# Kernel tuning notes

Measured on AMD Instinct MI355X. Metric: run time of the kernel, lower is better.

## Reference

```python
import jax, jax.numpy as jnp
import numpy as np

TOP_K = 2
NUM_EXPERTS = 8


def setup_inputs() -> dict:
    key = jax.random.key(0)
    ks = jax.random.split(key, 5)
    N, D, H, E = 32768, 1024, 1024, NUM_EXPERTS
    s = 1.0 / np.sqrt(D)
    return {
        "x": jax.random.normal(ks[0], (N, D), dtype=jnp.float32),
        "router_w": jax.random.normal(ks[1], (E, D), dtype=jnp.float32) * s,
        "router_b": jax.random.normal(ks[2], (E,), dtype=jnp.float32) * s,
        "expert_w": jax.random.normal(ks[3], (E, D, H), dtype=jnp.float32) * s,
        "expert_b": jax.random.normal(ks[4], (E, H), dtype=jnp.float32) * s,
    }


def reference(x, router_w, router_b, expert_w, expert_b):
    # Router: torch Linear -> x @ W.T + b ; logits [N, E]
    logits = x @ router_w.T + router_b
    vals, idx = jax.lax.top_k(logits, TOP_K)          # [N, K]
    w = jax.nn.softmax(vals, axis=-1)                  # softmax over top-k values
    # combine[n, e] = sum of top-k weights routed to expert e (0 if not chosen)
    combine = jnp.sum(jax.nn.one_hot(idx, NUM_EXPERTS, dtype=x.dtype) * w[..., None], axis=1)  # [N, E]
    # Accumulate weighted expert outputs; unchosen tokens get combine==0,
    # which matches the torch masking (bias excluded for unchosen tokens).
    out = jnp.zeros((x.shape[0], expert_w.shape[2]), dtype=x.dtype)
    for e in range(NUM_EXPERTS):
        out = out + combine[:, e:e + 1] * (x @ expert_w[e] + expert_b[e])
    return out
```

## Files before the change

### kernel.cpp

```cpp
#include <hip/hip_runtime.h>
#include <hip/hip_bf16.h>
#include <math.h>

#define N_TOK 32768
#define DIM   1024
#define HID   1024
#define NE    8
#define GX    64

typedef __bf16 bf16_t;
typedef __bf16 bf16x8 __attribute__((ext_vector_type(8)));
typedef __bf16 bf16x4 __attribute__((ext_vector_type(4)));
typedef float  f32x4  __attribute__((ext_vector_type(4)));

#define GLOAD_LDS(g, s) __builtin_amdgcn_global_load_lds(                      \
    (const __attribute__((address_space(1))) void*)(g),                        \
    (__attribute__((address_space(3))) void*)(s), 16, 0, 0)

__global__ __launch_bounds__(256) void convert_w_kernel(const float* __restrict__ W,
                                                        bf16_t* __restrict__ Wt) {
  __shared__ float tile[64][65];
  const int e  = blockIdx.z;
  const int d0 = blockIdx.x * 64;
  const int h0 = blockIdx.y * 64;
  const int t  = threadIdx.x;
  const float* src = W + (size_t)e * DIM * HID;
#pragma unroll
  for (int p = 0; p < 4; ++p) {
    int r = p * 16 + (t >> 4);
    int c = (t & 15) * 4;
    f32x4 v = *(const f32x4*)&src[(size_t)(d0 + r) * HID + h0 + c];
    tile[r][c + 0] = v[0]; tile[r][c + 1] = v[1];
    tile[r][c + 2] = v[2]; tile[r][c + 3] = v[3];
  }
  __syncthreads();
  const int hr = t >> 2, dseg = t & 3;
  bf16_t tmp[16];
#pragma unroll
  for (int j = 0; j < 16; ++j) tmp[j] = (bf16_t)tile[dseg * 16 + j][hr];
  bf16_t* dst = Wt + (size_t)e * HID * DIM + (size_t)(h0 + hr) * DIM + d0 + dseg * 16;
  *(bf16x8*)dst       = *(const bf16x8*)tmp;
  *(bf16x8*)(dst + 8) = *(const bf16x8*)(tmp + 8);
}

__global__ __launch_bounds__(256) void router_kernel(
    const float* __restrict__ x, const float* __restrict__ rw,
    const float* __restrict__ rb, bf16_t* __restrict__ xb,
    int* __restrict__ tok_list, float* __restrict__ w_list,
    int* __restrict__ gcnt) {
  __shared__ float rws[NE * DIM];
  __shared__ int   ce0[64], ce1[64];
  __shared__ float cw0[64], cw1[64];
  __shared__ int   lp0[64], lp1[64];
  __shared__ int   lcnt[2 * NE], gbase[2 * NE];
  const int t = threadIdx.x;
#pragma unroll
  for (int p = 0; p < 8; ++p) {
    int i4 = p * 256 + t;
    *(f32x4*)&rws[i4 * 4] = *(const f32x4*)&rw[i4 * 4];
  }
  if (t < 2 * NE) lcnt[t] = 0;
  __syncthreads();

  const int w = t >> 6, l = t & 63, ts = l >> 4, sub = l & 15;
  const int base = blockIdx.x * 64;
  for (int it = 0; it < 4; ++it) {
    const int lt    = it * 16 + w * 4 + ts;
    const int token = base + lt;
    const float* xrow  = x  + (size_t)token * DIM;
    bf16_t*      xbrow = xb + (size_t)token * DIM;
    double acc[NE];
#pragma unroll
    for (int e = 0; e < NE; ++e) acc[e] = 0.0;
    for (int p = 0; p < 16; ++p) {
      const int d = p * 64 + sub * 4;
      f32x4 xv = *(const f32x4*)&xrow[d];
      bf16x4 bv;
#pragma unroll
      for (int j = 0; j < 4; ++j) bv[j] = (bf16_t)xv[j];
      *(bf16x4*)&xbrow[d] = bv;
#pragma unroll
      for (int e = 0; e < NE; ++e) {
        f32x4 rv = *(const f32x4*)&rws[e * DIM + d];
        acc[e] += (double)xv[0] * (double)rv[0] + (double)xv[1] * (double)rv[1]
                + (double)xv[2] * (double)rv[2] + (double)xv[3] * (double)rv[3];
      }
    }
#pragma unroll
    for (int e = 0; e < NE; ++e) {
      double v = acc[e];
      v += __shfl_xor(v, 1, 16);
      v += __shfl_xor(v, 2, 16);
      v += __shfl_xor(v, 4, 16);
      v += __shfl_xor(v, 8, 16);
      acc[e] = v;
    }
    if (sub == 0) {
      double lv[NE];
#pragma unroll
      for (int e = 0; e < NE; ++e) lv[e] = acc[e] + (double)rb[e];
      int e0 = 0; double v0 = lv[0];
#pragma unroll
      for (int e = 1; e < NE; ++e) if (lv[e] > v0) { v0 = lv[e]; e0 = e; }
      int e1 = -1; double v1 = -1.0e300;
#pragma unroll
      for (int e = 0; e < NE; ++e) if (e != e0 && lv[e] > v1) { v1 = lv[e]; e1 = e; }
      const float ef = expf((float)(v1 - v0));
      const float s  = 1.0f + ef;
      ce0[lt] = e0; ce1[lt] = e1;
      cw0[lt] = 1.0f / s; cw1[lt] = ef / s;
    }
  }
  __syncthreads();
  if (t < 64) {
    lp0[t] = atomicAdd(&lcnt[ce0[t] * 2 + 0], 1);
    lp1[t] = atomicAdd(&lcnt[ce1[t] * 2 + 1], 1);
  }
  __syncthreads();
  if (t < 2 * NE) gbase[t] = atomicAdd(&gcnt[t], lcnt[t]);
  __syncthreads();
  if (t < 64) {
    const int token = base + t;
    const int le0 = ce0[t] * 2 + 0, le1 = ce1[t] * 2 + 1;
    const int p0 = gbase[le0] + lp0[t];
    const int p1 = gbase[le1] + lp1[t];
    tok_list[le0 * N_TOK + p0] = token;  w_list[le0 * N_TOK + p0] = cw0[t];
    tok_list[le1 * N_TOK + p1] = token;  w_list[le1 * N_TOK + p1] = cw1[t];
  }
}

#define BM 128
#define BN 128
#define BK 32

__global__ __launch_bounds__(256) void moe_gemm_kernel(
    const bf16_t* __restrict__ xb, const bf16_t* __restrict__ wt,
    const float* __restrict__ eb, const int* __restrict__ tok_list,
    const float* __restrict__ w_list, const int* __restrict__ gcnt,
    float* __restrict__ out, int slot) {
  const int f  = blockIdx.x + GX * (blockIdx.y + (HID / BN) * blockIdx.z);
  const int wg = (f & 7) * (GX * (HID / BN) * NE / 8) + (f >> 3);
  const int bx = wg % GX;
  const int by = (wg / GX) % (HID / BN);
  const int e  = wg / (GX * (HID / BN));

  const int le = e * 2 + slot;
  const int c  = gcnt[le];
  const int m0 = bx * BM;
  if (m0 >= c) return;
  const int h0 = by * BN;

  __shared__ bf16_t As[BM * BK];
  __shared__ bf16_t Bs[BN * BK];
  __shared__ int    tok_s[BM];
  __shared__ float  w_s[BM];

  const int t = threadIdx.x;
  if (t < BM) {
    int r  = m0 + t;
    int rc = r < c ? r : c - 1;
    tok_s[t] = tok_list[le * N_TOK + rc];
    w_s[t]   = (r < c) ? w_list[le * N_TOK + r] : 0.0f;
  }
  __syncthreads();

  const int w  = t >> 6, l = t & 63;
  const int wr = w >> 1, wc = w & 1;
  const int srow = t >> 2, sslot = t & 3;
  const int sx = (sslot ^ (srow & 3)) * 8;

  const bf16_t* ag0 = xb + (size_t)tok_s[srow] * DIM + sx;
  const bf16_t* ag1 = xb + (size_t)tok_s[srow + 64] * DIM + sx;
  const bf16_t* wbase = wt + (size_t)e * HID * DIM;
  const bf16_t* bg0 = wbase + (size_t)(h0 + srow) * DIM + sx;
  const bf16_t* bg1 = wbase + (size_t)(h0 + srow + 64) * DIM + sx;

  f32x4 acc[4][4];
  const f32x4 fzero = {0.0f, 0.0f, 0.0f, 0.0f};
#pragma unroll
  for (int m = 0; m < 4; ++m)
#pragma unroll
    for (int n = 0; n < 4; ++n) acc[m][n] = fzero;

  const int fr = l & 15, fq = l >> 4;
  const int rdx = (fq ^ (fr & 3)) * 8;

  for (int k0 = 0; k0 < DIM; k0 += BK) {
    GLOAD_LDS(ag0 + k0, As + w * 512);
    GLOAD_LDS(ag1 + k0, As + 2048 + w * 512);
    GLOAD_LDS(bg0 + k0, Bs + w * 512);
    GLOAD_LDS(bg1 + k0, Bs + 2048 + w * 512);
    __syncthreads();

    bf16x8 af[4], bfg[4];
#pragma unroll
    for (int m = 0; m < 4; ++m)
      af[m] = *(const bf16x8*)&As[(wr * 64 + m * 16 + fr) * BK + rdx];
#pragma unroll
    for (int n = 0; n < 4; ++n)
      bfg[n] = *(const bf16x8*)&Bs[(wc * 64 + n * 16 + fr) * BK + rdx];
#pragma unroll
    for (int m = 0; m < 4; ++m)
#pragma unroll
      for (int n = 0; n < 4; ++n)
        acc[m][n] = __builtin_amdgcn_mfma_f32_16x16x32_bf16(af[m], bfg[n],
                                                            acc[m][n], 0, 0, 0);
    __syncthreads();
  }

#pragma unroll
  for (int n = 0; n < 4; ++n) {
    const int h    = h0 + wc * 64 + n * 16 + fr;
    const float bias = eb[e * HID + h];
#pragma unroll
    for (int m = 0; m < 4; ++m) {
#pragma unroll
      for (int q = 0; q < 4; ++q) {
        const int r  = wr * 64 + m * 16 + fq * 4 + q;
        const float wv = w_s[r];
        if (wv != 0.0f) {
          const size_t o = (size_t)tok_s[r] * HID + h;
          const float  v = wv * (acc[m][n][q] + bias);
          if (slot == 0) out[o] = v;
          else           out[o] = out[o] + v;
        }
      }
    }
  }
}

extern "C" void kernel_launch(void* const* d_in, const int* in_sizes, int n_in,
                              void* d_out, int out_size, void* d_ws, size_t ws_size,
                              hipStream_t stream) {
  const float* x  = (const float*)d_in[0];
  const float* rw = (const float*)d_in[1];
  const float* rb = (const float*)d_in[2];
  const float* ew = (const float*)d_in[3];
  const float* eb = (const float*)d_in[4];
  float* out = (float*)d_out;

  char* ws = (char*)d_ws;
  bf16_t* xb       = (bf16_t*)(ws);
  bf16_t* wt       = (bf16_t*)(ws + 67108864);
  int*    tok_list = (int*)   (ws + 83886080);
  float*  w_list   = (float*) (ws + 85983232);
  int*    gcnt     = (int*)   (ws + 88080384);

  hipMemsetAsync(gcnt, 0, 2 * NE * sizeof(int), stream);

  convert_w_kernel<<<dim3(DIM / 64, HID / 64, NE), 256, 0, stream>>>(ew, wt);
  router_kernel<<<dim3(N_TOK / 64), 256, 0, stream>>>(x, rw, rb, xb,
                                                      tok_list, w_list, gcnt);

  dim3 grid(GX, HID / BN, NE);
  moe_gemm_kernel<<<grid, 256, 0, stream>>>(xb, wt, eb, tok_list, w_list, gcnt,
                                            out, 0);
  moe_gemm_kernel<<<grid, 256, 0, stream>>>(xb, wt, eb, tok_list, w_list, gcnt,
                                            out, 1);
}
```

Baseline: 577.8 us.

## Enlarge MoE GEMM tiles to 256x256 with a double-buffered async LDS pipeline

Rewrites the grouped expert GEMM to use 256x256 output tiles with BK=64, 512 threads and a 128KB dynamic LDS double buffer. Async global-to-LDS loads are issued in quarter-tile steps ahead of the MFMA work and tracked with explicit vmcnt waits and raw barriers. s_setprio is raised around the MFMA bursts. The aim is more data reuse per tile and less load latency exposed between k-steps. The cost is higher register and LDS pressure, and only one workgroup may fit per CU.

```diff
diff --git a/kernel.cpp b/kernel.cpp
--- a/kernel.cpp
+++ b/kernel.cpp
@@ -6,7 +6,6 @@
 #define DIM   1024
 #define HID   1024
 #define NE    8
-#define GX    64
 
 typedef __bf16 bf16_t;
 typedef __bf16 bf16x8 __attribute__((ext_vector_type(8)));
@@ -16,6 +15,9 @@
 #define GLOAD_LDS(g, s) __builtin_amdgcn_global_load_lds(                      \
     (const __attribute__((address_space(1))) void*)(g),                        \
     (__attribute__((address_space(3))) void*)(s), 16, 0, 0)
+
+#define BARRIER() do { __builtin_amdgcn_s_barrier();                           \
+                       asm volatile("" ::: "memory"); } while (0)
 
 __global__ __launch_bounds__(256) void convert_w_kernel(const float* __restrict__ W,
                                                         bf16_t* __restrict__ Wt) {
@@ -129,20 +131,39 @@
   }
 }
 
-#define BM 128
-#define BN 128
-#define BK 32
-
-__global__ __launch_bounds__(256) void moe_gemm_kernel(
+#define BM 256
+#define BN 256
+#define BK 64
+#define NT (DIM / BK)
+#define GX 32
+
+#define MF(x, y, m, n) acc[m][n] = \
+    __builtin_amdgcn_mfma_f32_16x16x32_bf16((x), (y), acc[m][n], 0, 0, 0)
+
+#define MFMA16(MB) do {                                                        \
+    __builtin_amdgcn_s_setprio(1);                                             \
+    MF(a0, b0, (MB)+0, 0); MF(a0, b1, (MB)+0, 1);                              \
+    MF(a0, b2, (MB)+0, 2); MF(a0, b3, (MB)+0, 3);                              \
+    MF(a1, b0, (MB)+1, 0); MF(a1, b1, (MB)+1, 1);                              \
+    MF(a1, b2, (MB)+1, 2); MF(a1, b3, (MB)+1, 3);                              \
+    MF(a2, b0, (MB)+2, 0); MF(a2, b1, (MB)+2, 1);                              \
+    MF(a2, b2, (MB)+2, 2); MF(a2, b3, (MB)+2, 3);                              \
+    MF(a3, b0, (MB)+3, 0); MF(a3, b1, (MB)+3, 1);                              \
+    MF(a3, b2, (MB)+3, 2); MF(a3, b3, (MB)+3, 3);                              \
+    __builtin_amdgcn_s_setprio(0);                                             \
+  } while (0)
+
+__global__ __launch_bounds__(512, 2) void moe_gemm_kernel(
     const bf16_t* __restrict__ xb, const bf16_t* __restrict__ wt,
     const float* __restrict__ eb, const int* __restrict__ tok_list,
     const float* __restrict__ w_list, const int* __restrict__ gcnt,
     float* __restrict__ out, int slot) {
-  const int f  = blockIdx.x + GX * (blockIdx.y + (HID / BN) * blockIdx.z);
+  const int f  = blockIdx.x;
   const int wg = (f & 7) * (GX * (HID / BN) * NE / 8) + (f >> 3);
-  const int bx = wg % GX;
-  const int by = (wg / GX) % (HID / BN);
   const int e  = wg / (GX * (HID / BN));
+  const int rr = wg % (GX * (HID / BN));
+  const int bx = rr >> 2;
+  const int by = rr & 3;
 
   const int le = e * 2 + slot;
   const int c  = gcnt[le];
@@ -150,10 +171,9 @@
   if (m0 >= c) return;
   const int h0 = by * BN;
 
-  __shared__ bf16_t As[BM * BK];
-  __shared__ bf16_t Bs[BN * BK];
-  __shared__ int    tok_s[BM];
-  __shared__ float  w_s[BM];
+  extern __shared__ bf16_t lds[];
+  __shared__ int   tok_s[BM];
+  __shared__ float w_s[BM];
 
   const int t = threadIdx.x;
   if (t < BM) {
@@ -164,63 +184,118 @@
   }
   __syncthreads();
 
+  const int srow = t >> 2, sslot = t & 3;
+  const int sswz = (sslot ^ ((srow >> 1) & 3)) * 8;
+  const bf16_t* wbase = wt + (size_t)e * HID * DIM;
+  const bf16_t* aR0 = xb + (size_t)tok_s[srow] * DIM + sswz;
+  const bf16_t* aR1 = xb + (size_t)tok_s[srow + 128] * DIM + sswz;
+  const bf16_t* bR0 = wbase + (size_t)(h0 + srow) * DIM + sswz;
+  const bf16_t* bR1 = wbase + (size_t)(h0 + srow + 128) * DIM + sswz;
+
+  auto stage_half = [&](int s_) {
+    if (s_ < 4 * NT) {
+      const int tile_ = s_ >> 2;
+      const int typ_  = s_ & 3;
+      const int buf_  = tile_ & 1;
+      const int kk_   = typ_ >> 1;
+      const int koff_ = tile_ * BK + kk_ * 32;
+      bf16_t* db_ = lds + ((typ_ & 1) ? 32768 : 0) + buf_ * 16384 + kk_ * 8192
+                        + t * 8;
+      if (typ_ & 1) { GLOAD_LDS(bR0 + koff_, db_); GLOAD_LDS(bR1 + koff_, db_ + 4096); }
+      else          { GLOAD_LDS(aR0 + koff_, db_); GLOAD_LDS(aR1 + koff_, db_ + 4096); }
+    }
+  };
+
   const int w  = t >> 6, l = t & 63;
-  const int wr = w >> 1, wc = w & 1;
-  const int srow = t >> 2, sslot = t & 3;
-  const int sx = (sslot ^ (srow & 3)) * 8;
-
-  const bf16_t* ag0 = xb + (size_t)tok_s[srow] * DIM + sx;
-  const bf16_t* ag1 = xb + (size_t)tok_s[srow + 64] * DIM + sx;
-  const bf16_t* wbase = wt + (size_t)e * HID * DIM;
-  const bf16_t* bg0 = wbase + (size_t)(h0 + srow) * DIM + sx;
-  const bf16_t* bg1 = wbase + (size_t)(h0 + srow + 64) * DIM + sx;
-
-  f32x4 acc[4][4];
+  const int wr = w >> 2, wc = w & 3;
+  const int fr = l & 15, fq = l >> 4;
+  const int rswz = (fq ^ ((fr >> 1) & 3)) * 8;
+  const int aoff = (wr * 128 + fr) * 32 + rswz;
+  const int boff = (wc * 64 + fr) * 32 + rswz;
+
+  f32x4 acc[8][4];
   const f32x4 fzero = {0.0f, 0.0f, 0.0f, 0.0f};
 #pragma unroll
-  for (int m = 0; m < 4; ++m)
+  for (int m = 0; m < 8; ++m)
 #pragma unroll
     for (int n = 0; n < 4; ++n) acc[m][n] = fzero;
 
-  const int fr = l & 15, fq = l >> 4;
-  const int rdx = (fq ^ (fr & 3)) * 8;
-
-  for (int k0 = 0; k0 < DIM; k0 += BK) {
-    GLOAD_LDS(ag0 + k0, As + w * 512);
-    GLOAD_LDS(ag1 + k0, As + 2048 + w * 512);
-    GLOAD_LDS(bg0 + k0, Bs + w * 512);
-    GLOAD_LDS(bg1 + k0, Bs + 2048 + w * 512);
-    __syncthreads();
-
-    bf16x8 af[4], bfg[4];
-#pragma unroll
-    for (int m = 0; m < 4; ++m)
-      af[m] = *(const bf16x8*)&As[(wr * 64 + m * 16 + fr) * BK + rdx];
-#pragma unroll
-    for (int n = 0; n < 4; ++n)
-      bfg[n] = *(const bf16x8*)&Bs[(wc * 64 + n * 16 + fr) * BK + rdx];
-#pragma unroll
-    for (int m = 0; m < 4; ++m)
-#pragma unroll
-      for (int n = 0; n < 4; ++n)
-        acc[m][n] = __builtin_amdgcn_mfma_f32_16x16x32_bf16(af[m], bfg[n],
-                                                            acc[m][n], 0, 0, 0);
-    __syncthreads();
-  }
-
-#pragma unroll
-  for (int n = 0; n < 4; ++n) {
-    const int h    = h0 + wc * 64 + n * 16 + fr;
+  stage_half(0); stage_half(1); stage_half(2); stage_half(3);
+  stage_half(4); stage_half(5); stage_half(6);
+  asm volatile("s_waitcnt vmcnt(6)" ::: "memory");
+  BARRIER();
+  int s = 7;
+
+#pragma unroll 2
+  for (int kt = 0; kt < NT; ++kt) {
+    const int buf = kt & 1;
+    const bf16_t* Ab0 = lds + buf * 16384;
+    const bf16_t* Ab1 = Ab0 + 8192;
+    const bf16_t* Bb0 = lds + 32768 + buf * 16384;
+    const bf16_t* Bb1 = Bb0 + 8192;
+    bf16x8 a0, a1, a2, a3, b0, b1, b2, b3;
+
+    a0 = *(const bf16x8*)(Ab0 + aoff + 0 * 512);
+    a1 = *(const bf16x8*)(Ab0 + aoff + 1 * 512);
+    a2 = *(const bf16x8*)(Ab0 + aoff + 2 * 512);
+    a3 = *(const bf16x8*)(Ab0 + aoff + 3 * 512);
+    b0 = *(const bf16x8*)(Bb0 + boff + 0 * 512);
+    b1 = *(const bf16x8*)(Bb0 + boff + 1 * 512);
+    b2 = *(const bf16x8*)(Bb0 + boff + 2 * 512);
+    b3 = *(const bf16x8*)(Bb0 + boff + 3 * 512);
+    stage_half(s + 0);
+    BARRIER();
+    MFMA16(0);
+    BARRIER();
+
+    a0 = *(const bf16x8*)(Ab0 + aoff + 4 * 512);
+    a1 = *(const bf16x8*)(Ab0 + aoff + 5 * 512);
+    a2 = *(const bf16x8*)(Ab0 + aoff + 6 * 512);
+    a3 = *(const bf16x8*)(Ab0 + aoff + 7 * 512);
+    stage_half(s + 1);
+    BARRIER();
+    MFMA16(4);
+    BARRIER();
+
+    a0 = *(const bf16x8*)(Ab1 + aoff + 0 * 512);
+    a1 = *(const bf16x8*)(Ab1 + aoff + 1 * 512);
+    a2 = *(const bf16x8*)(Ab1 + aoff + 2 * 512);
+    a3 = *(const bf16x8*)(Ab1 + aoff + 3 * 512);
+    b0 = *(const bf16x8*)(Bb1 + boff + 0 * 512);
+    b1 = *(const bf16x8*)(Bb1 + boff + 1 * 512);
+    b2 = *(const bf16x8*)(Bb1 + boff + 2 * 512);
+    b3 = *(const bf16x8*)(Bb1 + boff + 3 * 512);
+    stage_half(s + 2);
+    BARRIER();
+    MFMA16(0);
+    BARRIER();
+
+    a0 = *(const bf16x8*)(Ab1 + aoff + 4 * 512);
+    a1 = *(const bf16x8*)(Ab1 + aoff + 5 * 512);
+    a2 = *(const bf16x8*)(Ab1 + aoff + 6 * 512);
+    a3 = *(const bf16x8*)(Ab1 + aoff + 7 * 512);
+    stage_half(s + 3);
+    BARRIER();
+    MFMA16(4);
+    if (kt < NT - 2)       asm volatile("s_waitcnt vmcnt(6)" ::: "memory");
+    else if (kt == NT - 2) asm volatile("s_waitcnt vmcnt(0)" ::: "memory");
+    BARRIER();
+    s += 4;
+  }
+
+#pragma unroll
+  for (int nf = 0; nf < 4; ++nf) {
+    const int h = h0 + wc * 64 + nf * 16 + fr;
     const float bias = eb[e * HID + h];
 #pragma unroll
-    for (int m = 0; m < 4; ++m) {
+    for (int mf = 0; mf < 8; ++mf) {
 #pragma unroll
       for (int q = 0; q < 4; ++q) {
-        const int r  = wr * 64 + m * 16 + fq * 4 + q;
+        const int r = wr * 128 + mf * 16 + fq * 4 + q;
         const float wv = w_s[r];
         if (wv != 0.0f) {
           const size_t o = (size_t)tok_s[r] * HID + h;
-          const float  v = wv * (acc[m][n][q] + bias);
+          const float v = wv * (acc[mf][nf][q] + bias);
           if (slot == 0) out[o] = v;
           else           out[o] = out[o] + v;
         }
@@ -252,9 +327,11 @@
   router_kernel<<<dim3(N_TOK / 64), 256, 0, stream>>>(x, rw, rb, xb,
                                                       tok_list, w_list, gcnt);
 
-  dim3 grid(GX, HID / BN, NE);
-  moe_gemm_kernel<<<grid, 256, 0, stream>>>(xb, wt, eb, tok_list, w_list, gcnt,
-                                            out, 0);
-  moe_gemm_kernel<<<grid, 256, 0, stream>>>(xb, wt, eb, tok_list, w_list, gcnt,
-                                            out, 1);
+  hipFuncSetAttribute((const void*)moe_gemm_kernel,
+                      hipFuncAttributeMaxDynamicSharedMemorySize, 131072);
+  const int nwg = GX * (HID / BN) * NE;
+  moe_gemm_kernel<<<nwg, 512, 131072, stream>>>(xb, wt, eb, tok_list, w_list,
+                                                gcnt, out, 0);
+  moe_gemm_kernel<<<nwg, 512, 131072, stream>>>(xb, wt, eb, tok_list, w_list,
+                                                gcnt, out, 1);
 }
```

New measurement: 630.2 us. 9.1% more time.
